# Kernel tuning notes

Hardware: AMD Instinct MI355X
Metric: run time of the kernel (lower is better)

Reference implementation:

```python
import jax, jax.numpy as jnp
import numpy as np

NUM_GRAPHS = 8192
NODES_PER_GRAPH = 128
TOTAL_NODES = NUM_GRAPHS * NODES_PER_GRAPH
C = 128


def setup_inputs() -> dict:
    key = jax.random.key(0)
    k1, k2, k3 = jax.random.split(key, 3)
    x = jax.random.normal(k1, (TOTAL_NODES, C), dtype=jnp.float32)
    # sorted graph-id assignment; every graph id 0..B-1 appears
    batch = (jnp.arange(TOTAL_NODES, dtype=jnp.int64) // NODES_PER_GRAPH)
    W = jax.random.normal(k2, (C, C), dtype=jnp.float32) * (1.0 / np.sqrt(C))
    b = jax.random.normal(k3, (C,), dtype=jnp.float32) * 0.01
    return {"x": x, "batch": batch, "W": W, "b": b}


def reference(x, batch, W, b):
    # to_dense_batch(x, batch)[0][:, 0] == first node of each graph.
    # batch is sorted, so first occurrence of graph g is searchsorted(batch, g).
    num_graphs = NUM_GRAPHS
    first_idx = jnp.searchsorted(batch, jnp.arange(num_graphs, dtype=batch.dtype))
    pooled = x[first_idx]                      # [B, C]
    return pooled @ W.T + b                    # nn.Linear: x W^T + b
```

## Files before the change

### kernel.cpp

```cpp
#include <hip/hip_runtime.h>
#include <stdint.h>

#define NUM_GRAPHS 8192
#define NODES_PER_GRAPH 128
#define TOTAL_NODES (NUM_GRAPHS * NODES_PER_GRAPH)
#define C 128

typedef __attribute__((ext_vector_type(8))) short bf16x8;
typedef __attribute__((ext_vector_type(4))) float f32x4;

static __device__ __forceinline__ short f2bf(float f) {
    union { float f; uint32_t u; } v; v.f = f;
    const uint32_t u = v.u;
    return (short)((u + 0x7fffu + ((u >> 16) & 1u)) >> 16);
}

__global__ void first_occ_kernel(const int* __restrict__ batch, int* __restrict__ fidx) {
    const int i = blockIdx.x * blockDim.x + threadIdx.x;
    if (i >= TOTAL_NODES) return;
    const int b = batch[i];
    if ((i == 0 || batch[i - 1] != b) && (unsigned)b < (unsigned)NUM_GRAPHS)
        fidx[b] = i;
}

__global__ __launch_bounds__(64) void pool_linear_kernel(
        const float* __restrict__ x, const float* __restrict__ W,
        const float* __restrict__ bias, const int* __restrict__ fidx,
        float* __restrict__ out) {
    const int l  = threadIdx.x;
    const int r  = l & 15;
    const int kg = l >> 4;
    const int gbase = blockIdx.x * 16;

    const int fi = fidx[gbase + r];
    const float* xrow = x + (size_t)fi * C;
    bf16x8 a[4];
#pragma unroll
    for (int kc = 0; kc < 4; ++kc) {
        const int k0 = kc * 32 + kg * 8;
        const float4 lo = *reinterpret_cast<const float4*>(xrow + k0);
        const float4 hi = *reinterpret_cast<const float4*>(xrow + k0 + 4);
        a[kc][0] = f2bf(lo.x); a[kc][1] = f2bf(lo.y); a[kc][2] = f2bf(lo.z); a[kc][3] = f2bf(lo.w);
        a[kc][4] = f2bf(hi.x); a[kc][5] = f2bf(hi.y); a[kc][6] = f2bf(hi.z); a[kc][7] = f2bf(hi.w);
    }

#pragma unroll
    for (int ct = 0; ct < 8; ++ct) {
        const int col = ct * 16 + r;
        const float* wrow = W + (size_t)col * C;
        const float bc = bias[col];
        f32x4 acc = {bc, bc, bc, bc};
#pragma unroll
        for (int kc = 0; kc < 4; ++kc) {
            const int k0 = kc * 32 + kg * 8;
            const float4 lo = *reinterpret_cast<const float4*>(wrow + k0);
            const float4 hi = *reinterpret_cast<const float4*>(wrow + k0 + 4);
            bf16x8 bf;
            bf[0] = f2bf(lo.x); bf[1] = f2bf(lo.y); bf[2] = f2bf(lo.z); bf[3] = f2bf(lo.w);
            bf[4] = f2bf(hi.x); bf[5] = f2bf(hi.y); bf[6] = f2bf(hi.z); bf[7] = f2bf(hi.w);
            acc = __builtin_amdgcn_mfma_f32_16x16x32_bf16(a[kc], bf, acc, 0, 0, 0);
        }
#pragma unroll
        for (int reg = 0; reg < 4; ++reg) {
            const int row = gbase + kg * 4 + reg;
            out[(size_t)row * C + col] = acc[reg];
        }
    }
}

extern "C" void kernel_launch(void* const* d_in, const int* in_sizes, int n_in,
                              void* d_out, int out_size, void* d_ws, size_t ws_size,
                              hipStream_t stream) {
    const float* x     = (const float*)d_in[0];
    const int*   batch = (const int*)d_in[1];
    const float* W     = (const float*)d_in[2];
    const float* b     = (const float*)d_in[3];
    float*       out   = (float*)d_out;
    int*         fidx  = (int*)d_ws;

    first_occ_kernel<<<TOTAL_NODES / 256, 256, 0, stream>>>(batch, fidx);
    pool_linear_kernel<<<NUM_GRAPHS / 16, 64, 0, stream>>>(x, W, b, fidx, out);
}
```

Before: 16.01 us.

## Vectorize first-occurrence scan and split output columns across more blocks

The first-occurrence kernel now loads four batch ids per thread with an int4 load and launches a quarter of the threads. The pool+linear kernel splits the 8 output column tiles across 4 blocks per 16-graph group, so there are 2048 blocks instead of 512. This is meant to raise occupancy and parallelism on a small grid. The cost is that each gathered x row is loaded and converted four times instead of once.

Result: slower. 16.85 us (+5.2%).

```diff
diff --git a/kernel.cpp b/kernel.cpp
--- a/kernel.cpp
+++ b/kernel.cpp
@@ -5,6 +5,8 @@
 #define NODES_PER_GRAPH 128
 #define TOTAL_NODES (NUM_GRAPHS * NODES_PER_GRAPH)
 #define C 128
+#define GGROUPS (NUM_GRAPHS / 16)
+#define CSPLIT 4
 
 typedef __attribute__((ext_vector_type(8))) short bf16x8;
 typedef __attribute__((ext_vector_type(4))) float f32x4;
@@ -15,22 +17,30 @@
     return (short)((u + 0x7fffu + ((u >> 16) & 1u)) >> 16);
 }
 
-__global__ void first_occ_kernel(const int* __restrict__ batch, int* __restrict__ fidx) {
-    const int i = blockIdx.x * blockDim.x + threadIdx.x;
-    if (i >= TOTAL_NODES) return;
-    const int b = batch[i];
-    if ((i == 0 || batch[i - 1] != b) && (unsigned)b < (unsigned)NUM_GRAPHS)
-        fidx[b] = i;
+__global__ __launch_bounds__(256) void first_occ_kernel(
+        const int* __restrict__ batch, int* __restrict__ fidx) {
+    const int i4 = blockIdx.x * blockDim.x + threadIdx.x;
+    const int base = i4 * 4;
+    const int4 v = *reinterpret_cast<const int4*>(batch + base);
+    const int prev = (base == 0) ? -1 : batch[base - 1];
+    if (v.x != prev && (unsigned)v.x < NUM_GRAPHS) fidx[v.x] = base;
+    if (v.y != v.x  && (unsigned)v.y < NUM_GRAPHS) fidx[v.y] = base + 1;
+    if (v.z != v.y  && (unsigned)v.z < NUM_GRAPHS) fidx[v.z] = base + 2;
+    if (v.w != v.z  && (unsigned)v.w < NUM_GRAPHS) fidx[v.w] = base + 3;
 }
 
 __global__ __launch_bounds__(64) void pool_linear_kernel(
         const float* __restrict__ x, const float* __restrict__ W,
         const float* __restrict__ bias, const int* __restrict__ fidx,
         float* __restrict__ out) {
+    const int bid = blockIdx.x;
+    const int gg  = bid & (GGROUPS - 1);
+    const int cth = bid >> 9;
+
     const int l  = threadIdx.x;
     const int r  = l & 15;
     const int kg = l >> 4;
-    const int gbase = blockIdx.x * 16;
+    const int gbase = gg * 16;
 
     const int fi = fidx[gbase + r];
     const float* xrow = x + (size_t)fi * C;
@@ -45,7 +55,8 @@
     }
 
 #pragma unroll
-    for (int ct = 0; ct < 8; ++ct) {
+    for (int t = 0; t < 2; ++t) {
+        const int ct  = cth * 2 + t;
         const int col = ct * 16 + r;
         const float* wrow = W + (size_t)col * C;
         const float bc = bias[col];
@@ -78,6 +89,6 @@
     float*       out   = (float*)d_out;
     int*         fidx  = (int*)d_ws;
 
-    first_occ_kernel<<<TOTAL_NODES / 256, 256, 0, stream>>>(batch, fidx);
-    pool_linear_kernel<<<NUM_GRAPHS / 16, 64, 0, stream>>>(x, W, b, fidx, out);
+    first_occ_kernel<<<TOTAL_NODES / 4 / 256, 256, 0, stream>>>(batch, fidx);
+    pool_linear_kernel<<<CSPLIT * GGROUPS, 64, 0, stream>>>(x, W, b, fidx, out);
 }
```
